# Kernel tuning notes

Measured on AMD Instinct MI355X. Metric: run time of the kernel, lower is better.

Reference implementation:

```python
import jax, jax.numpy as jnp
import numpy as np

N = 50000
E = 800000
F0, F1, F2 = 256, 128, 64
EPS = 1e-5


def setup_inputs() -> dict:
    key = jax.random.key(0)
    ks = jax.random.split(key, 20)
    x = jax.random.normal(ks[0], (N, F0), dtype=jnp.float32)
    src = jax.random.randint(ks[1], (E,), 0, N)
    dst = jax.random.randint(ks[2], (E,), 0, N)
    edge_index = jnp.stack([src, dst]).astype(jnp.int64)

    def lin(k, fi, fo):
        s = 1.0 / np.sqrt(fi)
        k1, k2 = jax.random.split(k)
        W = jax.random.uniform(k1, (fi, fo), minval=-s, maxval=s, dtype=jnp.float32)
        b = jax.random.uniform(k2, (fo,), minval=-s, maxval=s, dtype=jnp.float32)
        return W, b

    We1, be1 = lin(ks[3], F0, F1)
    We2, be2 = lin(ks[4], F1, F2)
    Wd1, bd1 = lin(ks[5], F2, F1)
    Wd2, bd2 = lin(ks[6], F1, F0)
    return {
        'x': x, 'edge_index': edge_index,
        'We1': We1, 'be1': be1, 'g1': jnp.ones((F1,)), 'bb1': jnp.zeros((F1,)),
        'We2': We2, 'be2': be2, 'g2': jnp.ones((F2,)), 'bb2': jnp.zeros((F2,)),
        'Wd1': Wd1, 'bd1': bd1, 'g3': jnp.ones((F1,)), 'bb3': jnp.zeros((F1,)),
        'Wd2': Wd2, 'bd2': bd2, 'g4': jnp.ones((F0,)), 'bb4': jnp.zeros((F0,)),
    }


def _gcn(x, W, b, src, dst, dinv_src_dst, dinv_self):
    # PyG GCNConv: linear first, then sym-normalized propagation with self-loops
    h = x @ W + b                               # [N, Fout]
    msg = h[src] * dinv_src_dst[:, None]        # [E, Fout]
    out = jax.ops.segment_sum(msg, dst, num_segments=N)
    return out + h * dinv_self[:, None]         # self-loop term


def _bn(x, g, b):
    # BatchNorm1d training-mode: biased batch stats over node dim
    m = jnp.mean(x, axis=0)
    v = jnp.mean(jnp.square(x - m), axis=0)
    return g * (x - m) * jax.lax.rsqrt(v + EPS) + b


def reference(x, edge_index, We1, be1, g1, bb1, We2, be2, g2, bb2,
              Wd1, bd1, g3, bb3, Wd2, bd2, g4, bb4):
    src, dst = edge_index[0], edge_index[1]
    deg = jnp.zeros((N,), x.dtype).at[dst].add(1.0) + 1.0  # in-degree + self-loop
    dinv = jax.lax.rsqrt(deg)
    dsd = dinv[src] * dinv[dst]
    dself = dinv * dinv

    relu = jax.nn.relu
    # Encoder block 0 (outer i==0): relu(GCN), relu(BN)
    h = relu(_gcn(x, We1, be1, src, dst, dsd, dself))
    h = relu(_bn(h, g1, bb1))
    enc1 = h
    # Encoder block 1 (outer i==1 == len(inner)-1): relu(GCN), BN (no relu)
    h = relu(_gcn(h, We2, be2, src, dst, dsd, dself))
    h = _bn(h, g2, bb2)
    enc2 = h
    # Decoder block 0: relu(GCN), relu(BN)
    h = relu(_gcn(h, Wd1, bd1, src, dst, dsd, dself))
    h = relu(_bn(h, g3, bb3))
    # Decoder block 1 (i==1): relu(GCN), BN (no relu)
    h = relu(_gcn(h, Wd2, bd2, src, dst, dsd, dself))
    h = _bn(h, g4, bb4)
    # AE returns (reconstruction, encoded_embeddings)
    return h, enc1, enc2
```

## Files before the change

kernel.cpp:

```cpp
#include <hip/hip_runtime.h>

#define N_NODES 50000
#define F0 256
#define F1 128
#define F2 64
#define BN_EPS 1e-5f

typedef float f32x4 __attribute__((ext_vector_type(4)));
typedef __bf16 bf16x8 __attribute__((ext_vector_type(8)));
typedef unsigned short ushort8v __attribute__((ext_vector_type(8)));

__device__ __forceinline__ float bflo(unsigned v) { return __uint_as_float(v << 16); }
__device__ __forceinline__ float bfhi(unsigned v) { return __uint_as_float(v & 0xFFFF0000u); }
__device__ __forceinline__ unsigned short f2bf(float f) {
  unsigned u = __float_as_uint(f);
  u += 0x7FFFu + ((u >> 16) & 1u);
  return (unsigned short)(u >> 16);
}
__device__ __forceinline__ void split2(float a, unsigned short& hi, unsigned short& lo) {
  hi = f2bf(a);
  float hf = __uint_as_float((unsigned)hi << 16);
  lo = f2bf(a - hf);
}
__device__ __forceinline__ int rdl(int v, int l) { return __builtin_amdgcn_readlane(v, l); }
__device__ __forceinline__ float rdlf(float v, int l) {
  return __uint_as_float((unsigned)__builtin_amdgcn_readlane(__float_as_int(v), l));
}

__global__ void count_dst(const int* __restrict__ dst, int* __restrict__ counts, int E) {
  int e = blockIdx.x * blockDim.x + threadIdx.x;
  if (e < E) atomicAdd(&counts[dst[e]], 1);
}

__global__ __launch_bounds__(256) void scan_blocks(const int* __restrict__ counts,
                                                   int* __restrict__ offs,
                                                   int* __restrict__ bsum,
                                                   float* __restrict__ dinv) {
  __shared__ int s_w[4];
  const int tid = threadIdx.x, lane = tid & 63, wid = tid >> 6;
  const int base = blockIdx.x * 1024 + tid * 4;
  int v0 = 0, v1 = 0, v2 = 0, v3 = 0;
  if (base + 3 < N_NODES) {
    int4 v = *(const int4*)(counts + base);
    v0 = v.x; v1 = v.y; v2 = v.z; v3 = v.w;
  } else if (base < N_NODES) {
    v0 = counts[base];
    if (base + 1 < N_NODES) v1 = counts[base + 1];
    if (base + 2 < N_NODES) v2 = counts[base + 2];
  }
  if (base < N_NODES) {
    dinv[base] = rsqrtf((float)v0 + 1.0f);
    if (base + 1 < N_NODES) dinv[base + 1] = rsqrtf((float)v1 + 1.0f);
    if (base + 2 < N_NODES) dinv[base + 2] = rsqrtf((float)v2 + 1.0f);
    if (base + 3 < N_NODES) dinv[base + 3] = rsqrtf((float)v3 + 1.0f);
  }
  int t = v0 + v1 + v2 + v3;
  int incl = t;
#pragma unroll
  for (int d = 1; d < 64; d <<= 1) {
    int x = __shfl_up(incl, d);
    if (lane >= d) incl += x;
  }
  if (lane == 63) s_w[wid] = incl;
  __syncthreads();
  int woff = 0;
#pragma unroll
  for (int j = 0; j < 4; j++)
    if (j < wid) woff += s_w[j];
  int p = woff + incl - t;
  if (base < N_NODES) offs[base] = p;
  p += v0;
  if (base + 1 < N_NODES) offs[base + 1] = p;
  p += v1;
  if (base + 2 < N_NODES) offs[base + 2] = p;
  p += v2;
  if (base + 3 < N_NODES) offs[base + 3] = p;
  if (tid == 255) bsum[blockIdx.x] = woff + incl;
}

__global__ void scan_tops(int* __restrict__ bsum, int* __restrict__ offs, int nblk) {
  int lane = threadIdx.x;
  int v = (lane < nblk) ? bsum[lane] : 0;
  int incl = v;
#pragma unroll
  for (int d = 1; d < 64; d <<= 1) {
    int x = __shfl_up(incl, d);
    if (lane >= d) incl += x;
  }
  if (lane < nblk) bsum[lane] = incl - v;
  if (lane == 63) offs[N_NODES] = incl;
}

__global__ __launch_bounds__(256) void scan_add(int* __restrict__ offs,
                                                const int* __restrict__ bsum) {
  const int add = bsum[blockIdx.x];
  const int base = blockIdx.x * 1024 + threadIdx.x * 4;
  if (base + 3 < N_NODES) {
    int4 v = *(const int4*)(offs + base);
    v.x += add; v.y += add; v.z += add; v.w += add;
    *(int4*)(offs + base) = v;
  } else if (base < N_NODES) {
    offs[base] += add;
    if (base + 1 < N_NODES) offs[base + 1] += add;
    if (base + 2 < N_NODES) offs[base + 2] += add;
  }
}

__global__ void fill_csr(const int* __restrict__ src, const int* __restrict__ dst,
                         const int* __restrict__ offs, int* __restrict__ cursor,
                         const float* __restrict__ dinv,
                         int* __restrict__ csr_src, float* __restrict__ csr_w, int E) {
  int e = blockIdx.x * blockDim.x + threadIdx.x;
  if (e < E) {
    int s = src[e], d = dst[e];
    int p = offs[d] + atomicAdd(&cursor[d], 1);
    csr_src[p] = s;
    csr_w[p] = dinv[s] * dinv[d];
  }
}

__global__ void compute_rowsum(const int* __restrict__ offs, const float* __restrict__ csr_w,
                               const float* __restrict__ dinv, float* __restrict__ rowsum) {
  int i = blockIdx.x * blockDim.x + threadIdx.x;
  if (i < N_NODES) {
    float s = dinv[i] * dinv[i];
    int e1 = offs[i + 1];
    for (int e = offs[i]; e < e1; e++) s += csr_w[e];
    rowsum[i] = s;
  }
}

__device__ __forceinline__ void wt_one(const float* W, unsigned short* Wh, unsigned short* Wl,
                                       int K, int N, int idx) {
  int k = idx / N, n = idx - k * N;
  unsigned short h, l;
  split2(W[idx], h, l);
  Wh[(size_t)n * K + k] = h;
  Wl[(size_t)n * K + k] = l;
}

__global__ void convert_weights(const float* __restrict__ We1, const float* __restrict__ We2,
                                const float* __restrict__ Wd1, const float* __restrict__ Wd2,
                                unsigned short* W1h, unsigned short* W1l,
                                unsigned short* W2h, unsigned short* W2l,
                                unsigned short* W3h, unsigned short* W3l,
                                unsigned short* W4h, unsigned short* W4l) {
  int idx = blockIdx.x * blockDim.x + threadIdx.x;
  if (idx < 32768) {
    wt_one(We1, W1h, W1l, 256, 128, idx);
  } else if (idx < 40960) {
    wt_one(We2, W2h, W2l, 128, 64, idx - 32768);
  } else if (idx < 49152) {
    wt_one(Wd1, W3h, W3l, 64, 128, idx - 40960);
  } else if (idx < 81920) {
    wt_one(Wd2, W4h, W4l, 128, 256, idx - 49152);
  }
}

template <int BN, bool STATS, bool AF32>
__global__ __launch_bounds__(256) void mfma_gemm_split(
    const unsigned short* __restrict__ Ahi, const unsigned short* __restrict__ Alo,
    const float* __restrict__ Af,
    const unsigned short* __restrict__ Whi, const unsigned short* __restrict__ Wlo,
    const float* __restrict__ bias, const float* __restrict__ rowsum,
    unsigned short* __restrict__ Cb, float* __restrict__ Cf,
    float* __restrict__ stat, int M, int K, int N) {
  constexpr int BM = 128;
  constexpr int MT = (BN == 128) ? 4 : 2;
  constexpr int NT = 4;
  __shared__ __align__(16) unsigned short AsH[4][BM][8];
  __shared__ __align__(16) unsigned short AsL[4][BM][8];
  __shared__ __align__(16) unsigned short BsH[4][BN][8];
  __shared__ __align__(16) unsigned short BsL[4][BN][8];
  const int tid = threadIdx.x;
  const int lane = tid & 63, wid = tid >> 6;
  const int quad = lane >> 4, ln = lane & 15;
  const int m0 = blockIdx.x * BM;
  const int n0 = blockIdx.y * BN;
  const int wm = (BN == 128) ? (wid & 1) * 64 : wid * 32;
  const int wn = (BN == 128) ? (wid >> 1) * 64 : 0;
  f32x4 acc[MT][NT] = {};

  const int arow = tid >> 2, aseg = tid & 3;
  for (int k0 = 0; k0 < K; k0 += 32) {
#pragma unroll
    for (int i = 0; i < 2; i++) {
      int row = arow + i * 64;
      int gm = m0 + row;
      if (AF32) {
        float4 u0 = make_float4(0.f, 0.f, 0.f, 0.f), u1 = u0;
        if (gm < M) {
          u0 = *(const float4*)(Af + (size_t)gm * K + k0 + aseg * 8);
          u1 = *(const float4*)(Af + (size_t)gm * K + k0 + aseg * 8 + 4);
        }
        ushort4 h0, l0, h1, l1;
        split2(u0.x, h0.x, l0.x); split2(u0.y, h0.y, l0.y);
        split2(u0.z, h0.z, l0.z); split2(u0.w, h0.w, l0.w);
        split2(u1.x, h1.x, l1.x); split2(u1.y, h1.y, l1.y);
        split2(u1.z, h1.z, l1.z); split2(u1.w, h1.w, l1.w);
        *(ushort4*)(&AsH[aseg][row][0]) = h0;
        *(ushort4*)(&AsH[aseg][row][4]) = h1;
        *(ushort4*)(&AsL[aseg][row][0]) = l0;
        *(ushort4*)(&AsL[aseg][row][4]) = l1;
      } else {
        ushort8v vh = {0, 0, 0, 0, 0, 0, 0, 0};
        ushort8v vl = {0, 0, 0, 0, 0, 0, 0, 0};
        if (gm < M) {
          vh = *(const ushort8v*)(Ahi + (size_t)gm * K + k0 + aseg * 8);
          vl = *(const ushort8v*)(Alo + (size_t)gm * K + k0 + aseg * 8);
        }
        *(ushort8v*)(&AsH[aseg][row][0]) = vh;
        *(ushort8v*)(&AsL[aseg][row][0]) = vl;
      }
    }
#pragma unroll
    for (int i = 0; i < BN / 64; i++) {
      int n = arow + i * 64;
      *(ushort8v*)(&BsH[aseg][n][0]) =
          *(const ushort8v*)(Whi + (size_t)(n0 + n) * K + k0 + aseg * 8);
      *(ushort8v*)(&BsL[aseg][n][0]) =
          *(const ushort8v*)(Wlo + (size_t)(n0 + n) * K + k0 + aseg * 8);
    }
    __syncthreads();
    bf16x8 ah[MT], al[MT], bh[NT], bl[NT];
#pragma unroll
    for (int mt = 0; mt < MT; mt++) {
      ah[mt] = *(const bf16x8*)(&AsH[quad][wm + mt * 16 + ln][0]);
      al[mt] = *(const bf16x8*)(&AsL[quad][wm + mt * 16 + ln][0]);
    }
#pragma unroll
    for (int nt = 0; nt < NT; nt++) {
      bh[nt] = *(const bf16x8*)(&BsH[quad][wn + nt * 16 + ln][0]);
      bl[nt] = *(const bf16x8*)(&BsL[quad][wn + nt * 16 + ln][0]);
    }
#pragma unroll
    for (int mt = 0; mt < MT; mt++)
#pragma unroll
      for (int nt = 0; nt < NT; nt++) {
        acc[mt][nt] = __builtin_amdgcn_mfma_f32_16x16x32_bf16(ah[mt], bl[nt], acc[mt][nt], 0, 0, 0);
        acc[mt][nt] = __builtin_amdgcn_mfma_f32_16x16x32_bf16(al[mt], bh[nt], acc[mt][nt], 0, 0, 0);
        acc[mt][nt] = __builtin_amdgcn_mfma_f32_16x16x32_bf16(ah[mt], bh[nt], acc[mt][nt], 0, 0, 0);
      }
    __syncthreads();
  }

  if (!STATS) {
#pragma unroll
    for (int nt = 0; nt < NT; nt++) {
      int gn = n0 + wn + nt * 16 + ln;
      float bv = bias[gn];
#pragma unroll
      for (int mt = 0; mt < MT; mt++) {
#pragma unroll
        for (int r = 0; r < 4; r++) {
          int gm = m0 + wm + mt * 16 + quad * 4 + r;
          if (gm < M) Cb[(size_t)gm * N + gn] = f2bf(acc[mt][nt][r] + bv);
        }
      }
    }
  } else {
    float rs[MT][4];
#pragma unroll
    for (int mt = 0; mt < MT; mt++)
#pragma unroll
      for (int r = 0; r < 4; r++) {
        int gm = m0 + wm + mt * 16 + quad * 4 + r;
        rs[mt][r] = (gm < M) ? rowsum[gm] : 0.f;
      }
#pragma unroll
    for (int nt = 0; nt < NT; nt++) {
      int gn = n0 + wn + nt * 16 + ln;
      float bv = bias[gn];
      float ls = 0.f, lq = 0.f;
#pragma unroll
      for (int mt = 0; mt < MT; mt++) {
#pragma unroll
        for (int r = 0; r < 4; r++) {
          int gm = m0 + wm + mt * 16 + quad * 4 + r;
          if (gm < M) {
            float v = fmaxf(fmaf(bv, rs[mt][r], acc[mt][nt][r]), 0.f);
            Cf[(size_t)gm * N + gn] = v;
            ls += v;
            lq = fmaf(v, v, lq);
          }
        }
      }
      ls += __shfl_xor(ls, 16); ls += __shfl_xor(ls, 32);
      lq += __shfl_xor(lq, 16); lq += __shfl_xor(lq, 32);
      if (quad == 0) {
        atomicAdd(&stat[gn], ls);
        atomicAdd(&stat[256 + gn], lq);
      }
    }
  }
}

template <bool RELU_STATS, bool OUT_SPLIT>
__global__ __launch_bounds__(256) void agg128_rl(
    const unsigned short* __restrict__ hb, const int* __restrict__ offs,
    const int* __restrict__ csr_src, const float* __restrict__ csr_w,
    const float* __restrict__ dinv, float* __restrict__ outf,
    unsigned short* __restrict__ outhi, unsigned short* __restrict__ outlo,
    float* __restrict__ stat) {
  const int tid = threadIdx.x;
  const int lane = tid & 63;
  const int widx = tid >> 6;
  const int half = lane >> 5;
  const int hl = lane & 31;
  const int nwaves = gridDim.x * 4;
  float ls0 = 0.f, ls1 = 0.f, ls2 = 0.f, ls3 = 0.f;
  float lq0 = 0.f, lq1 = 0.f, lq2 = 0.f, lq3 = 0.f;

  for (int node = blockIdx.x * 4 + widx; node < N_NODES; node += nwaves) {
    const int e0 = __builtin_amdgcn_readfirstlane(offs[node]);
    const int e1 = __builtin_amdgcn_readfirstlane(offs[node + 1]);
    float a0 = 0.f, a1 = 0.f, a2 = 0.f, a3 = 0.f;
    for (int e = e0; e < e1; e += 64) {
      const int cnt = min(64, e1 - e);
      int idx = 0;
      float wt = 0.f;
      if (lane < cnt) {
        idx = csr_src[e + lane];
        wt = csr_w[e + lane];
      }
      const int nb = (cnt + 15) & ~15;
      for (int j = 0; j < nb; j += 16) {
#pragma unroll
        for (int u = 0; u < 8; u++) {
          int sa = rdl(idx, j + 2 * u);
          int sb = rdl(idx, j + 2 * u + 1);
          float wa = rdlf(wt, j + 2 * u);
          float wb = rdlf(wt, j + 2 * u + 1);
          int s = half ? sb : sa;
          float w = half ? wb : wa;
          uint2 v = *(const uint2*)(hb + (size_t)s * 128 + hl * 4);
          a0 = fmaf(bflo(v.x), w, a0);
          a1 = fmaf(bfhi(v.x), w, a1);
          a2 = fmaf(bflo(v.y), w, a2);
          a3 = fmaf(bfhi(v.y), w, a3);
        }
      }
    }
    a0 += __shfl_xor(a0, 32);
    a1 += __shfl_xor(a1, 32);
    a2 += __shfl_xor(a2, 32);
    a3 += __shfl_xor(a3, 32);
    float di = dinv[node];
    float ds = di * di;
    uint2 vs = *(const uint2*)(hb + (size_t)node * 128 + hl * 4);
    a0 = fmaf(bflo(vs.x), ds, a0);
    a1 = fmaf(bfhi(vs.x), ds, a1);
    a2 = fmaf(bflo(vs.y), ds, a2);
    a3 = fmaf(bfhi(vs.y), ds, a3);
    if (RELU_STATS) {
      a0 = fmaxf(a0, 0.f);
      a1 = fmaxf(a1, 0.f);
      a2 = fmaxf(a2, 0.f);
      a3 = fmaxf(a3, 0.f);
      if (half == 0) {
        ls0 += a0; ls1 += a1; ls2 += a2; ls3 += a3;
        lq0 = fmaf(a0, a0, lq0);
        lq1 = fmaf(a1, a1, lq1);
        lq2 = fmaf(a2, a2, lq2);
        lq3 = fmaf(a3, a3, lq3);
      }
    }
    if (half == 0) {
      if (OUT_SPLIT) {
        unsigned short h0, l0, h1, l1, h2, l2, h3, l3;
        split2(a0, h0, l0);
        split2(a1, h1, l1);
        split2(a2, h2, l2);
        split2(a3, h3, l3);
        ushort4 hv, lv;
        hv.x = h0; hv.y = h1; hv.z = h2; hv.w = h3;
        lv.x = l0; lv.y = l1; lv.z = l2; lv.w = l3;
        *(ushort4*)(outhi + (size_t)node * 128 + hl * 4) = hv;
        *(ushort4*)(outlo + (size_t)node * 128 + hl * 4) = lv;
      } else {
        *(float4*)(outf + (size_t)node * 128 + hl * 4) = make_float4(a0, a1, a2, a3);
      }
    }
  }

  if (RELU_STATS) {
    __shared__ float red[4][128];
    if (half == 0) {
      red[widx][hl * 4 + 0] = ls0;
      red[widx][hl * 4 + 1] = ls1;
      red[widx][hl * 4 + 2] = ls2;
      red[widx][hl * 4 + 3] = ls3;
    }
    __syncthreads();
    if (tid < 128) {
      atomicAdd(&stat[tid], red[0][tid] + red[1][tid] + red[2][tid] + red[3][tid]);
    }
    __syncthreads();
    if (half == 0) {
      red[widx][hl * 4 + 0] = lq0;
      red[widx][hl * 4 + 1] = lq1;
      red[widx][hl * 4 + 2] = lq2;
      red[widx][hl * 4 + 3] = lq3;
    }
    __syncthreads();
    if (tid < 128) {
      atomicAdd(&stat[256 + tid], red[0][tid] + red[1][tid] + red[2][tid] + red[3][tid]);
    }
  }
}

template <bool RELU_STATS, bool OUT_SPLIT>
__global__ __launch_bounds__(256) void agg64_rl(
    const unsigned short* __restrict__ hb, const int* __restrict__ offs,
    const int* __restrict__ csr_src, const float* __restrict__ csr_w,
    const float* __restrict__ dinv, float* __restrict__ outf,
    unsigned short* __restrict__ outhi, unsigned short* __restrict__ outlo,
    float* __restrict__ stat) {
  const int tid = threadIdx.x;
  const int lane = tid & 63;
  const int widx = tid >> 6;
  const int ql = lane & 15;
  const int nwaves = gridDim.x * 4;
  float ls0 = 0.f, ls1 = 0.f, ls2 = 0.f, ls3 = 0.f;
  float lq0 = 0.f, lq1 = 0.f, lq2 = 0.f, lq3 = 0.f;

  for (int node = blockIdx.x * 4 + widx; node < N_NODES; node += nwaves) {
    const int e0 = __builtin_amdgcn_readfirstlane(offs[node]);
    const int e1 = __builtin_amdgcn_readfirstlane(offs[node + 1]);
    float a0 = 0.f, a1 = 0.f, a2 = 0.f, a3 = 0.f;
    for (int e = e0; e < e1; e += 64) {
      const int cnt = min(64, e1 - e);
      int idx = 0;
      float wt = 0.f;
      if (lane < cnt) {
        idx = csr_src[e + lane];
        wt = csr_w[e + lane];
      }
      const int nb = (cnt + 31) & ~31;
      for (int j = 0; j < nb; j += 32) {
#pragma unroll
        for (int u = 0; u < 8; u++) {
          int s0 = rdl(idx, j + 4 * u + 0);
          int s1 = rdl(idx, j + 4 * u + 1);
          int s2 = rdl(idx, j + 4 * u + 2);
          int s3 = rdl(idx, j + 4 * u + 3);
          float w0 = rdlf(wt, j + 4 * u + 0);
          float w1 = rdlf(wt, j + 4 * u + 1);
          float w2 = rdlf(wt, j + 4 * u + 2);
          float w3 = rdlf(wt, j + 4 * u + 3);
          int sx = (lane & 16) ? s1 : s0;
          int sy = (lane & 16) ? s3 : s2;
          int s = (lane & 32) ? sy : sx;
          float wx = (lane & 16) ? w1 : w0;
          float wy = (lane & 16) ? w3 : w2;
          float w = (lane & 32) ? wy : wx;
          uint2 v = *(const uint2*)(hb + (size_t)s * 64 + ql * 4);
          a0 = fmaf(bflo(v.x), w, a0);
          a1 = fmaf(bfhi(v.x), w, a1);
          a2 = fmaf(bflo(v.y), w, a2);
          a3 = fmaf(bfhi(v.y), w, a3);
        }
      }
    }
    a0 += __shfl_xor(a0, 16); a0 += __shfl_xor(a0, 32);
    a1 += __shfl_xor(a1, 16); a1 += __shfl_xor(a1, 32);
    a2 += __shfl_xor(a2, 16); a2 += __shfl_xor(a2, 32);
    a3 += __shfl_xor(a3, 16); a3 += __shfl_xor(a3, 32);
    float di = dinv[node];
    float ds = di * di;
    uint2 vs = *(const uint2*)(hb + (size_t)node * 64 + ql * 4);
    a0 = fmaf(bflo(vs.x), ds, a0);
    a1 = fmaf(bfhi(vs.x), ds, a1);
    a2 = fmaf(bflo(vs.y), ds, a2);
    a3 = fmaf(bfhi(vs.y), ds, a3);
    if (RELU_STATS) {
      a0 = fmaxf(a0, 0.f);
      a1 = fmaxf(a1, 0.f);
      a2 = fmaxf(a2, 0.f);
      a3 = fmaxf(a3, 0.f);
      if (lane < 16) {
        ls0 += a0; ls1 += a1; ls2 += a2; ls3 += a3;
        lq0 = fmaf(a0, a0, lq0);
        lq1 = fmaf(a1, a1, lq1);
        lq2 = fmaf(a2, a2, lq2);
        lq3 = fmaf(a3, a3, lq3);
      }
    }
    if (lane < 16) {
      if (OUT_SPLIT) {
        unsigned short h0, l0, h1, l1, h2, l2, h3, l3;
        split2(a0, h0, l0);
        split2(a1, h1, l1);
        split2(a2, h2, l2);
        split2(a3, h3, l3);
        ushort4 hv, lv;
        hv.x = h0; hv.y = h1; hv.z = h2; hv.w = h3;
        lv.x = l0; lv.y = l1; lv.z = l2; lv.w = l3;
        *(ushort4*)(outhi + (size_t)node * 64 + ql * 4) = hv;
        *(ushort4*)(outlo + (size_t)node * 64 + ql * 4) = lv;
      } else {
        *(float4*)(outf + (size_t)node * 64 + ql * 4) = make_float4(a0, a1, a2, a3);
      }
    }
  }

  if (RELU_STATS) {
    __shared__ float red[4][64];
    if (lane < 16) {
      red[widx][ql * 4 + 0] = ls0;
      red[widx][ql * 4 + 1] = ls1;
      red[widx][ql * 4 + 2] = ls2;
      red[widx][ql * 4 + 3] = ls3;
    }
    __syncthreads();
    if (tid < 64) {
      atomicAdd(&stat[tid], red[0][tid] + red[1][tid] + red[2][tid] + red[3][tid]);
    }
    __syncthreads();
    if (lane < 16) {
      red[widx][ql * 4 + 0] = lq0;
      red[widx][ql * 4 + 1] = lq1;
      red[widx][ql * 4 + 2] = lq2;
      red[widx][ql * 4 + 3] = lq3;
    }
    __syncthreads();
    if (tid < 64) {
      atomicAdd(&stat[256 + tid], red[0][tid] + red[1][tid] + red[2][tid] + red[3][tid]);
    }
  }
}

template <int F, bool RELU, bool WF32, bool WB16, bool WSPLIT>
__global__ __launch_bounds__(256) void bn_apply_f(const float* __restrict__ a,
                                                  const float* __restrict__ stat,
                                                  const float* __restrict__ g,
                                                  const float* __restrict__ bb,
                                                  float* __restrict__ outf,
                                                  unsigned short* __restrict__ outb,
                                                  unsigned short* __restrict__ outhi,
                                                  unsigned short* __restrict__ outlo) {
  __shared__ float s_scale[F], s_shift[F];
  const int tid = threadIdx.x;
  if (tid < F) {
    const float invN = 1.0f / (float)N_NODES;
    float mean = stat[tid] * invN;
    float var = fmaxf(stat[256 + tid] * invN - mean * mean, 0.f);
    float inv = rsqrtf(var + BN_EPS);
    float sc = g[tid] * inv;
    s_scale[tid] = sc;
    s_shift[tid] = bb[tid] - mean * sc;
  }
  __syncthreads();
  constexpr int C4 = F / 4;
  const int total = N_NODES * C4;
  for (int idx = blockIdx.x * blockDim.x + tid; idx < total; idx += gridDim.x * blockDim.x) {
    int c4 = idx % C4;
    float4 v = ((const float4*)a)[idx];
    float4 s = *(float4*)&s_scale[c4 * 4];
    float4 sh = *(float4*)&s_shift[c4 * 4];
    float4 o;
    o.x = fmaf(v.x, s.x, sh.x);
    o.y = fmaf(v.y, s.y, sh.y);
    o.z = fmaf(v.z, s.z, sh.z);
    o.w = fmaf(v.w, s.w, sh.w);
    if (RELU) {
      o.x = fmaxf(o.x, 0.f);
      o.y = fmaxf(o.y, 0.f);
      o.z = fmaxf(o.z, 0.f);
      o.w = fmaxf(o.w, 0.f);
    }
    if (WF32) ((float4*)outf)[idx] = o;
    if (WB16) {
      ushort4 b;
      b.x = f2bf(o.x); b.y = f2bf(o.y); b.z = f2bf(o.z); b.w = f2bf(o.w);
      ((ushort4*)outb)[idx] = b;
    }
    if (WSPLIT) {
      ushort4 h, l;
      split2(o.x, h.x, l.x);
      split2(o.y, h.y, l.y);
      split2(o.z, h.z, l.z);
      split2(o.w, h.w, l.w);
      ((ushort4*)outhi)[idx] = h;
      ((ushort4*)outlo)[idx] = l;
    }
  }
}

extern "C" void kernel_launch(void* const* d_in, const int* in_sizes, int n_in,
                              void* d_out, int out_size, void* d_ws, size_t ws_size,
                              hipStream_t stream) {
  const float* x = (const float*)d_in[0];
  const int* ei = (const int*)d_in[1];
  const int E = in_sizes[1] / 2;
  const int* src = ei;
  const int* dst = ei + E;
  const float* We1 = (const float*)d_in[2];  const float* be1 = (const float*)d_in[3];
  const float* g1  = (const float*)d_in[4];  const float* bb1 = (const float*)d_in[5];
  const float* We2 = (const float*)d_in[6];  const float* be2 = (const float*)d_in[7];
  const float* g2  = (const float*)d_in[8];  const float* bb2 = (const float*)d_in[9];
  const float* Wd1 = (const float*)d_in[10]; const float* bd1 = (const float*)d_in[11];
  const float* g3  = (const float*)d_in[12]; const float* bb3 = (const float*)d_in[13];
  const float* Wd2 = (const float*)d_in[14]; const float* bd2 = (const float*)d_in[15];
  const float* g4  = (const float*)d_in[16]; const float* bb4 = (const float*)d_in[17];

  float* out = (float*)d_out;
  char* ws = (char*)d_ws;
  unsigned short* A0b  = (unsigned short*)(ws + 0);
  unsigned short* A1b  = (unsigned short*)(ws + 12800000);
  unsigned short* C2b  = (unsigned short*)(ws + 32000000);
  unsigned short* G3hi = (unsigned short*)(ws + 0);
  unsigned short* G3lo = (unsigned short*)(ws + 6400000);
  unsigned short* D3b  = (unsigned short*)(ws + 12800000);
  unsigned short* G4hi = (unsigned short*)(ws + 0);
  unsigned short* G4lo = (unsigned short*)(ws + 25600000);
  unsigned short* Wb   = (unsigned short*)(ws + 48000000);
  unsigned short* W1h = Wb;            unsigned short* W1l = W1h + 32768;
  unsigned short* W2h = W1l + 32768;   unsigned short* W2l = W2h + 8192;
  unsigned short* W3h = W2l + 8192;    unsigned short* W3l = W3h + 8192;
  unsigned short* W4h = W3l + 8192;    unsigned short* W4l = W4h + 32768;
  float* B0f  = (float*)(ws + 51200000);
  int*   csrS   = (int*)(ws + 102400000);
  float* csrW   = (float*)(ws + 105600000);
  float* stat4  = (float*)(ws + 108800000);
  int*   bsum   = (int*)(ws + 108808192);
  int*   counts = (int*)(ws + 108810000);
  int*   cursor = (int*)(ws + 109010000);
  int*   offs   = (int*)(ws + 109210000);
  float* dinv   = (float*)(ws + 109410064);
  if (ws_size < 109604160) return;
  float* rowsum = (float*)cursor;

  float* enc1 = out + (size_t)N_NODES * F0;
  float* enc2 = enc1 + (size_t)N_NODES * F1;

  const int EB = (E + 255) / 256;
  const int AGG_GRID = 2048;
  const int MB = (N_NODES + 127) / 128;
  const int SCAN_B = (N_NODES + 1023) / 1024;

  convert_weights<<<320, 256, 0, stream>>>(We1, We2, Wd1, Wd2, W1h, W1l, W2h, W2l,
                                           W3h, W3l, W4h, W4l);
  hipMemsetAsync(counts, 0, 2 * N_NODES * sizeof(int) + 20000, stream);
  hipMemsetAsync(stat4, 0, 4 * 512 * sizeof(float), stream);
  count_dst<<<EB, 256, 0, stream>>>(dst, counts, E);
  scan_blocks<<<SCAN_B, 256, 0, stream>>>(counts, offs, bsum, dinv);
  scan_tops<<<1, 64, 0, stream>>>(bsum, offs, SCAN_B);
  scan_add<<<SCAN_B, 256, 0, stream>>>(offs, bsum);
  fill_csr<<<EB, 256, 0, stream>>>(src, dst, offs, cursor, dinv, csrS, csrW, E);
  compute_rowsum<<<(N_NODES + 255) / 256, 256, 0, stream>>>(offs, csrW, dinv, rowsum);

  mfma_gemm_split<128, false, true><<<dim3(MB, 1), 256, 0, stream>>>(
      nullptr, nullptr, x, W1h, W1l, be1, nullptr, A0b, nullptr, nullptr, N_NODES, F0, F1);
  agg128_rl<true, false><<<AGG_GRID, 256, 0, stream>>>(
      A0b, offs, csrS, csrW, dinv, B0f, nullptr, nullptr, stat4);
  bn_apply_f<F1, true, true, false, false><<<2048, 256, 0, stream>>>(
      B0f, stat4, g1, bb1, enc1, nullptr, nullptr, nullptr);

  mfma_gemm_split<64, false, true><<<dim3(MB, 1), 256, 0, stream>>>(
      nullptr, nullptr, enc1, W2h, W2l, be2, nullptr, A1b, nullptr, nullptr, N_NODES, F1, F2);
  agg64_rl<true, false><<<AGG_GRID, 256, 0, stream>>>(
      A1b, offs, csrS, csrW, dinv, B0f, nullptr, nullptr, stat4 + 512);
  bn_apply_f<F2, false, true, true, false><<<2048, 256, 0, stream>>>(
      B0f, stat4 + 512, g2, bb2, enc2, C2b, nullptr, nullptr);

  agg64_rl<false, true><<<AGG_GRID, 256, 0, stream>>>(
      C2b, offs, csrS, csrW, dinv, nullptr, G3hi, G3lo, nullptr);
  mfma_gemm_split<128, true, false><<<dim3(MB, 1), 256, 0, stream>>>(
      G3hi, G3lo, nullptr, W3h, W3l, bd1, rowsum, nullptr, B0f, stat4 + 1024, N_NODES, F2, F1);
  bn_apply_f<F1, true, false, true, false><<<2048, 256, 0, stream>>>(
      B0f, stat4 + 1024, g3, bb3, nullptr, D3b, nullptr, nullptr);

  agg128_rl<false, true><<<AGG_GRID, 256, 0, stream>>>(
      D3b, offs, csrS, csrW, dinv, nullptr, G4hi, G4lo, nullptr);
  mfma_gemm_split<128, true, false><<<dim3(MB, 2), 256, 0, stream>>>(
      G4hi, G4lo, nullptr, W4h, W4l, bd2, rowsum, nullptr, B0f, stat4 + 1536, N_NODES, F1, F0);
  bn_apply_f<F0, false, true, false, false><<<2048, 256, 0, stream>>>(
      B0f, stat4 + 1536, g4, bb4, out, nullptr, nullptr, nullptr);
}
```

Baseline: 642.6 us.

## Slice bf16 features into 8-wide column panels for cache-resident sparse aggregation

```diff
diff --git a/kernel.cpp b/kernel.cpp
--- a/kernel.cpp
+++ b/kernel.cpp
@@ -21,10 +21,6 @@
   hi = f2bf(a);
   float hf = __uint_as_float((unsigned)hi << 16);
   lo = f2bf(a - hf);
-}
-__device__ __forceinline__ int rdl(int v, int l) { return __builtin_amdgcn_readlane(v, l); }
-__device__ __forceinline__ float rdlf(float v, int l) {
-  return __uint_as_float((unsigned)__builtin_amdgcn_readlane(__float_as_int(v), l));
 }
 
 __global__ void count_dst(const int* __restrict__ dst, int* __restrict__ counts, int E) {
@@ -92,41 +88,39 @@
 }
 
 __global__ __launch_bounds__(256) void scan_add(int* __restrict__ offs,
-                                                const int* __restrict__ bsum) {
+                                                const int* __restrict__ bsum,
+                                                const float* __restrict__ dinv,
+                                                float* __restrict__ rowsum) {
   const int add = bsum[blockIdx.x];
   const int base = blockIdx.x * 1024 + threadIdx.x * 4;
   if (base + 3 < N_NODES) {
     int4 v = *(const int4*)(offs + base);
     v.x += add; v.y += add; v.z += add; v.w += add;
     *(int4*)(offs + base) = v;
+    float4 d = *(const float4*)(dinv + base);
+    float4 r;
+    r.x = d.x * d.x; r.y = d.y * d.y; r.z = d.z * d.z; r.w = d.w * d.w;
+    *(float4*)(rowsum + base) = r;
   } else if (base < N_NODES) {
-    offs[base] += add;
-    if (base + 1 < N_NODES) offs[base + 1] += add;
-    if (base + 2 < N_NODES) offs[base + 2] += add;
+    for (int k = 0; k < 4 && base + k < N_NODES; k++) {
+      offs[base + k] += add;
+      float d = dinv[base + k];
+      rowsum[base + k] = d * d;
+    }
   }
 }
 
 __global__ void fill_csr(const int* __restrict__ src, const int* __restrict__ dst,
                          const int* __restrict__ offs, int* __restrict__ cursor,
                          const float* __restrict__ dinv,
-                         int* __restrict__ csr_src, float* __restrict__ csr_w, int E) {
+                         int2* __restrict__ csrP, float* __restrict__ rowsum, int E) {
   int e = blockIdx.x * blockDim.x + threadIdx.x;
   if (e < E) {
     int s = src[e], d = dst[e];
     int p = offs[d] + atomicAdd(&cursor[d], 1);
-    csr_src[p] = s;
-    csr_w[p] = dinv[s] * dinv[d];
-  }
-}
-
-__global__ void compute_rowsum(const int* __restrict__ offs, const float* __restrict__ csr_w,
-                               const float* __restrict__ dinv, float* __restrict__ rowsum) {
-  int i = blockIdx.x * blockDim.x + threadIdx.x;
-  if (i < N_NODES) {
-    float s = dinv[i] * dinv[i];
-    int e1 = offs[i + 1];
-    for (int e = offs[i]; e < e1; e++) s += csr_w[e];
-    rowsum[i] = s;
+    float w = dinv[s] * dinv[d];
+    csrP[p] = make_int2(s, __float_as_int(w));
+    atomicAdd(&rowsum[d], w);
   }
 }
 
@@ -249,12 +243,14 @@
     for (int nt = 0; nt < NT; nt++) {
       int gn = n0 + wn + nt * 16 + ln;
       float bv = bias[gn];
+      const int slice = gn >> 3, wi = gn & 7;
+      unsigned short* cp = Cb + (size_t)slice * (N_NODES * 8) + wi;
 #pragma unroll
       for (int mt = 0; mt < MT; mt++) {
 #pragma unroll
         for (int r = 0; r < 4; r++) {
           int gm = m0 + wm + mt * 16 + quad * 4 + r;
-          if (gm < M) Cb[(size_t)gm * N + gn] = f2bf(acc[mt][nt][r] + bv);
+          if (gm < M) cp[(size_t)gm * 8] = f2bf(acc[mt][nt][r] + bv);
         }
       }
     }
@@ -295,250 +291,142 @@
   }
 }
 
+
 template <bool RELU_STATS, bool OUT_SPLIT>
-__global__ __launch_bounds__(256) void agg128_rl(
+__device__ __forceinline__ void agg_emit(int node, int s, int chunk, int F,
+                                         float a0, float a1,
+                                         const unsigned short* __restrict__ hbs,
+                                         const float* __restrict__ dinv,
+                                         float* __restrict__ outf,
+                                         unsigned short* __restrict__ outhi,
+                                         unsigned short* __restrict__ outlo,
+                                         float& ls0, float& ls1, float& lq0, float& lq1) {
+  float di = dinv[node];
+  float ds = di * di;
+  unsigned v = *(const unsigned*)(hbs + (size_t)node * 8 + chunk * 2);
+  a0 = fmaf(bflo(v), ds, a0);
+  a1 = fmaf(bfhi(v), ds, a1);
+  if (RELU_STATS) {
+    a0 = fmaxf(a0, 0.f);
+    a1 = fmaxf(a1, 0.f);
+    ls0 += a0; ls1 += a1;
+    lq0 = fmaf(a0, a0, lq0);
+    lq1 = fmaf(a1, a1, lq1);
+  }
+  size_t p = (size_t)node * F + s * 8 + chunk * 2;
+  if (OUT_SPLIT) {
+    unsigned short h0, l0, h1, l1;
+    split2(a0, h0, l0);
+    split2(a1, h1, l1);
+    *(unsigned*)(outhi + p) = (unsigned)h0 | ((unsigned)h1 << 16);
+    *(unsigned*)(outlo + p) = (unsigned)l0 | ((unsigned)l1 << 16);
+  } else {
+    *(float2*)(outf + p) = make_float2(a0, a1);
+  }
+}
+
+template <bool RELU_STATS, bool OUT_SPLIT, int S>
+__global__ __launch_bounds__(256) void agg_sl(
     const unsigned short* __restrict__ hb, const int* __restrict__ offs,
-    const int* __restrict__ csr_src, const float* __restrict__ csr_w,
-    const float* __restrict__ dinv, float* __restrict__ outf,
-    unsigned short* __restrict__ outhi, unsigned short* __restrict__ outlo,
-    float* __restrict__ stat) {
+    const int2* __restrict__ csrP, const float* __restrict__ dinv,
+    float* __restrict__ outf, unsigned short* __restrict__ outhi,
+    unsigned short* __restrict__ outlo, float* __restrict__ stat, int nb) {
   const int tid = threadIdx.x;
   const int lane = tid & 63;
   const int widx = tid >> 6;
-  const int half = lane >> 5;
-  const int hl = lane & 31;
-  const int nwaves = gridDim.x * 4;
-  float ls0 = 0.f, ls1 = 0.f, ls2 = 0.f, ls3 = 0.f;
-  float lq0 = 0.f, lq1 = 0.f, lq2 = 0.f, lq3 = 0.f;
-
-  for (int node = blockIdx.x * 4 + widx; node < N_NODES; node += nwaves) {
-    const int e0 = __builtin_amdgcn_readfirstlane(offs[node]);
-    const int e1 = __builtin_amdgcn_readfirstlane(offs[node + 1]);
-    float a0 = 0.f, a1 = 0.f, a2 = 0.f, a3 = 0.f;
-    for (int e = e0; e < e1; e += 64) {
-      const int cnt = min(64, e1 - e);
-      int idx = 0;
-      float wt = 0.f;
-      if (lane < cnt) {
-        idx = csr_src[e + lane];
-        wt = csr_w[e + lane];
-      }
-      const int nb = (cnt + 15) & ~15;
-      for (int j = 0; j < nb; j += 16) {
-#pragma unroll
-        for (int u = 0; u < 8; u++) {
-          int sa = rdl(idx, j + 2 * u);
-          int sb = rdl(idx, j + 2 * u + 1);
-          float wa = rdlf(wt, j + 2 * u);
-          float wb = rdlf(wt, j + 2 * u + 1);
-          int s = half ? sb : sa;
-          float w = half ? wb : wa;
-          uint2 v = *(const uint2*)(hb + (size_t)s * 128 + hl * 4);
-          a0 = fmaf(bflo(v.x), w, a0);
-          a1 = fmaf(bfhi(v.x), w, a1);
-          a2 = fmaf(bflo(v.y), w, a2);
-          a3 = fmaf(bfhi(v.y), w, a3);
+  const int slot = lane >> 2;
+  const int chunk = lane & 3;
+  const int s = blockIdx.x % S;
+  const int blk = blockIdx.x / S;
+  const int stride = nb * 4;
+  constexpr int F = S * 8;
+  const unsigned short* hbs = hb + (size_t)s * (N_NODES * 8);
+  float ls0 = 0.f, ls1 = 0.f, lq0 = 0.f, lq1 = 0.f;
+
+  for (int base = blk * 4 + widx; base < N_NODES; base += 2 * stride) {
+    const int nA = base, nB = base + stride;
+    const bool hasB = (nB < N_NODES);
+    int eA = __builtin_amdgcn_readfirstlane(offs[nA]);
+    const int eA1 = __builtin_amdgcn_readfirstlane(offs[nA + 1]);
+    int eB = 0, eB1 = 0;
+    if (hasB) {
+      eB = __builtin_amdgcn_readfirstlane(offs[nB]);
+      eB1 = __builtin_amdgcn_readfirstlane(offs[nB + 1]);
+    }
+    float aA0 = 0.f, aA1 = 0.f, aB0 = 0.f, aB1 = 0.f;
+    while (eA < eA1 || eB < eB1) {
+      if (eA < eA1) {
+        int ee = eA + slot;
+        if (ee < eA1) {
+          unsigned long long cw =
+              __builtin_nontemporal_load((const unsigned long long*)&csrP[ee]);
+          int sn = (int)(unsigned)cw;
+          float w = __uint_as_float((unsigned)(cw >> 32));
+          unsigned v = *(const unsigned*)(hbs + (size_t)sn * 8 + chunk * 2);
+          aA0 = fmaf(bflo(v), w, aA0);
+          aA1 = fmaf(bfhi(v), w, aA1);
         }
       }
-    }
-    a0 += __shfl_xor(a0, 32);
-    a1 += __shfl_xor(a1, 32);
-    a2 += __shfl_xor(a2, 32);
-    a3 += __shfl_xor(a3, 32);
-    float di = dinv[node];
-    float ds = di * di;
-    uint2 vs = *(const uint2*)(hb + (size_t)node * 128 + hl * 4);
-    a0 = fmaf(bflo(vs.x), ds, a0);
-    a1 = fmaf(bfhi(vs.x), ds, a1);
-    a2 = fmaf(bflo(vs.y), ds, a2);
-    a3 = fmaf(bfhi(vs.y), ds, a3);
-    if (RELU_STATS) {
-      a0 = fmaxf(a0, 0.f);
-      a1 = fmaxf(a1, 0.f);
-      a2 = fmaxf(a2, 0.f);
-      a3 = fmaxf(a3, 0.f);
-      if (half == 0) {
-        ls0 += a0; ls1 += a1; ls2 += a2; ls3 += a3;
-        lq0 = fmaf(a0, a0, lq0);
-        lq1 = fmaf(a1, a1, lq1);
-        lq2 = fmaf(a2, a2, lq2);
-        lq3 = fmaf(a3, a3, lq3);
-      }
-    }
-    if (half == 0) {
-      if (OUT_SPLIT) {
-        unsigned short h0, l0, h1, l1, h2, l2, h3, l3;
-        split2(a0, h0, l0);
-        split2(a1, h1, l1);
-        split2(a2, h2, l2);
-        split2(a3, h3, l3);
-        ushort4 hv, lv;
-        hv.x = h0; hv.y = h1; hv.z = h2; hv.w = h3;
-        lv.x = l0; lv.y = l1; lv.z = l2; lv.w = l3;
-        *(ushort4*)(outhi + (size_t)node * 128 + hl * 4) = hv;
-        *(ushort4*)(outlo + (size_t)node * 128 + hl * 4) = lv;
-      } else {
-        *(float4*)(outf + (size_t)node * 128 + hl * 4) = make_float4(a0, a1, a2, a3);
-      }
+      if (eB < eB1) {
+        int ee = eB + slot;
+        if (ee < eB1) {
+          unsigned long long cw =
+              __builtin_nontemporal_load((const unsigned long long*)&csrP[ee]);
+          int sn = (int)(unsigned)cw;
+          float w = __uint_as_float((unsigned)(cw >> 32));
+          unsigned v = *(const unsigned*)(hbs + (size_t)sn * 8 + chunk * 2);
+          aB0 = fmaf(bflo(v), w, aB0);
+          aB1 = fmaf(bfhi(v), w, aB1);
+        }
+      }
+      eA += 16;
+      eB += 16;
+    }
+#pragma unroll
+    for (int d = 4; d < 64; d <<= 1) {
+      aA0 += __shfl_xor(aA0, d);
+      aA1 += __shfl_xor(aA1, d);
+    }
+    if (hasB) {
+#pragma unroll
+      for (int d = 4; d < 64; d <<= 1) {
+        aB0 += __shfl_xor(aB0, d);
+        aB1 += __shfl_xor(aB1, d);
+      }
+    }
+    if (slot == 0) {
+      agg_emit<RELU_STATS, OUT_SPLIT>(nA, s, chunk, F, aA0, aA1, hbs, dinv, outf, outhi, outlo,
+                                      ls0, ls1, lq0, lq1);
+      if (hasB)
+        agg_emit<RELU_STATS, OUT_SPLIT>(nB, s, chunk, F, aB0, aB1, hbs, dinv, outf, outhi, outlo,
+                                        ls0, ls1, lq0, lq1);
     }
   }
 
   if (RELU_STATS) {
-    __shared__ float red[4][128];
-    if (half == 0) {
-      red[widx][hl * 4 + 0] = ls0;
-      red[widx][hl * 4 + 1] = ls1;
-      red[widx][hl * 4 + 2] = ls2;
-      red[widx][hl * 4 + 3] = ls3;
+    __shared__ float red[4][16];
+    if (slot == 0) {
+      red[widx][chunk * 2 + 0] = ls0;
+      red[widx][chunk * 2 + 1] = ls1;
+      red[widx][8 + chunk * 2 + 0] = lq0;
+      red[widx][8 + chunk * 2 + 1] = lq1;
     }
     __syncthreads();
-    if (tid < 128) {
-      atomicAdd(&stat[tid], red[0][tid] + red[1][tid] + red[2][tid] + red[3][tid]);
-    }
-    __syncthreads();
-    if (half == 0) {
-      red[widx][hl * 4 + 0] = lq0;
-      red[widx][hl * 4 + 1] = lq1;
-      red[widx][hl * 4 + 2] = lq2;
-      red[widx][hl * 4 + 3] = lq3;
-    }
-    __syncthreads();
-    if (tid < 128) {
-      atomicAdd(&stat[256 + tid], red[0][tid] + red[1][tid] + red[2][tid] + red[3][tid]);
-    }
-  }
-}
-
-template <bool RELU_STATS, bool OUT_SPLIT>
-__global__ __launch_bounds__(256) void agg64_rl(
-    const unsigned short* __restrict__ hb, const int* __restrict__ offs,
-    const int* __restrict__ csr_src, const float* __restrict__ csr_w,
-    const float* __restrict__ dinv, float* __restrict__ outf,
-    unsigned short* __restrict__ outhi, unsigned short* __restrict__ outlo,
-    float* __restrict__ stat) {
-  const int tid = threadIdx.x;
-  const int lane = tid & 63;
-  const int widx = tid >> 6;
-  const int ql = lane & 15;
-  const int nwaves = gridDim.x * 4;
-  float ls0 = 0.f, ls1 = 0.f, ls2 = 0.f, ls3 = 0.f;
-  float lq0 = 0.f, lq1 = 0.f, lq2 = 0.f, lq3 = 0.f;
-
-  for (int node = blockIdx.x * 4 + widx; node < N_NODES; node += nwaves) {
-    const int e0 = __builtin_amdgcn_readfirstlane(offs[node]);
-    const int e1 = __builtin_amdgcn_readfirstlane(offs[node + 1]);
-    float a0 = 0.f, a1 = 0.f, a2 = 0.f, a3 = 0.f;
-    for (int e = e0; e < e1; e += 64) {
-      const int cnt = min(64, e1 - e);
-      int idx = 0;
-      float wt = 0.f;
-      if (lane < cnt) {
-        idx = csr_src[e + lane];
-        wt = csr_w[e + lane];
-      }
-      const int nb = (cnt + 31) & ~31;
-      for (int j = 0; j < nb; j += 32) {
-#pragma unroll
-        for (int u = 0; u < 8; u++) {
-          int s0 = rdl(idx, j + 4 * u + 0);
-          int s1 = rdl(idx, j + 4 * u + 1);
-          int s2 = rdl(idx, j + 4 * u + 2);
-          int s3 = rdl(idx, j + 4 * u + 3);
-          float w0 = rdlf(wt, j + 4 * u + 0);
-          float w1 = rdlf(wt, j + 4 * u + 1);
-          float w2 = rdlf(wt, j + 4 * u + 2);
-          float w3 = rdlf(wt, j + 4 * u + 3);
-          int sx = (lane & 16) ? s1 : s0;
-          int sy = (lane & 16) ? s3 : s2;
-          int s = (lane & 32) ? sy : sx;
-          float wx = (lane & 16) ? w1 : w0;
-          float wy = (lane & 16) ? w3 : w2;
-          float w = (lane & 32) ? wy : wx;
-          uint2 v = *(const uint2*)(hb + (size_t)s * 64 + ql * 4);
-          a0 = fmaf(bflo(v.x), w, a0);
-          a1 = fmaf(bfhi(v.x), w, a1);
-          a2 = fmaf(bflo(v.y), w, a2);
-          a3 = fmaf(bfhi(v.y), w, a3);
-        }
-      }
-    }
-    a0 += __shfl_xor(a0, 16); a0 += __shfl_xor(a0, 32);
-    a1 += __shfl_xor(a1, 16); a1 += __shfl_xor(a1, 32);
-    a2 += __shfl_xor(a2, 16); a2 += __shfl_xor(a2, 32);
-    a3 += __shfl_xor(a3, 16); a3 += __shfl_xor(a3, 32);
-    float di = dinv[node];
-    float ds = di * di;
-    uint2 vs = *(const uint2*)(hb + (size_t)node * 64 + ql * 4);
-    a0 = fmaf(bflo(vs.x), ds, a0);
-    a1 = fmaf(bfhi(vs.x), ds, a1);
-    a2 = fmaf(bflo(vs.y), ds, a2);
-    a3 = fmaf(bfhi(vs.y), ds, a3);
-    if (RELU_STATS) {
-      a0 = fmaxf(a0, 0.f);
-      a1 = fmaxf(a1, 0.f);
-      a2 = fmaxf(a2, 0.f);
-      a3 = fmaxf(a3, 0.f);
-      if (lane < 16) {
-        ls0 += a0; ls1 += a1; ls2 += a2; ls3 += a3;
-        lq0 = fmaf(a0, a0, lq0);
-        lq1 = fmaf(a1, a1, lq1);
-        lq2 = fmaf(a2, a2, lq2);
-        lq3 = fmaf(a3, a3, lq3);
-      }
-    }
-    if (lane < 16) {
-      if (OUT_SPLIT) {
-        unsigned short h0, l0, h1, l1, h2, l2, h3, l3;
-        split2(a0, h0, l0);
-        split2(a1, h1, l1);
-        split2(a2, h2, l2);
-        split2(a3, h3, l3);
-        ushort4 hv, lv;
-        hv.x = h0; hv.y = h1; hv.z = h2; hv.w = h3;
-        lv.x = l0; lv.y = l1; lv.z = l2; lv.w = l3;
-        *(ushort4*)(outhi + (size_t)node * 64 + ql * 4) = hv;
-        *(ushort4*)(outlo + (size_t)node * 64 + ql * 4) = lv;
-      } else {
-        *(float4*)(outf + (size_t)node * 64 + ql * 4) = make_float4(a0, a1, a2, a3);
-      }
-    }
-  }
-
-  if (RELU_STATS) {
-    __shared__ float red[4][64];
-    if (lane < 16) {
-      red[widx][ql * 4 + 0] = ls0;
-      red[widx][ql * 4 + 1] = ls1;
-      red[widx][ql * 4 + 2] = ls2;
-      red[widx][ql * 4 + 3] = ls3;
-    }
-    __syncthreads();
-    if (tid < 64) {
-      atomicAdd(&stat[tid], red[0][tid] + red[1][tid] + red[2][tid] + red[3][tid]);
-    }
-    __syncthreads();
-    if (lane < 16) {
-      red[widx][ql * 4 + 0] = lq0;
-      red[widx][ql * 4 + 1] = lq1;
-      red[widx][ql * 4 + 2] = lq2;
-      red[widx][ql * 4 + 3] = lq3;
-    }
-    __syncthreads();
-    if (tid < 64) {
-      atomicAdd(&stat[256 + tid], red[0][tid] + red[1][tid] + red[2][tid] + red[3][tid]);
-    }
-  }
-}
-
-template <int F, bool RELU, bool WF32, bool WB16, bool WSPLIT>
+    if (tid < 16) {
+      float v = red[0][tid] + red[1][tid] + red[2][tid] + red[3][tid];
+      int f = s * 8 + (tid & 7);
+      atomicAdd(&stat[(tid >> 3) * 256 + f], v);
+    }
+  }
+}
+
+template <int F, bool RELU, bool WF32, bool WB16>
 __global__ __launch_bounds__(256) void bn_apply_f(const float* __restrict__ a,
                                                   const float* __restrict__ stat,
                                                   const float* __restrict__ g,
                                                   const float* __restrict__ bb,
                                                   float* __restrict__ outf,
-                                                  unsigned short* __restrict__ outb,
-                                                  unsigned short* __restrict__ outhi,
-                                                  unsigned short* __restrict__ outlo) {
+                                                  unsigned short* __restrict__ outb) {
   __shared__ float s_scale[F], s_shift[F];
   const int tid = threadIdx.x;
   if (tid < F) {
@@ -555,6 +443,7 @@
   const int total = N_NODES * C4;
   for (int idx = blockIdx.x * blockDim.x + tid; idx < total; idx += gridDim.x * blockDim.x) {
     int c4 = idx % C4;
+    int node = idx / C4;
     float4 v = ((const float4*)a)[idx];
     float4 s = *(float4*)&s_scale[c4 * 4];
     float4 sh = *(float4*)&s_shift[c4 * 4];
@@ -573,16 +462,8 @@
     if (WB16) {
       ushort4 b;
       b.x = f2bf(o.x); b.y = f2bf(o.y); b.z = f2bf(o.z); b.w = f2bf(o.w);
-      ((ushort4*)outb)[idx] = b;
-    }
-    if (WSPLIT) {
-      ushort4 h, l;
-      split2(o.x, h.x, l.x);
-      split2(o.y, h.y, l.y);
-      split2(o.z, h.z, l.z);
-      split2(o.w, h.w, l.w);
-      ((ushort4*)outhi)[idx] = h;
-      ((ushort4*)outlo)[idx] = l;
+      int slice = c4 >> 1, half = c4 & 1;
+      ((ushort4*)outb)[(size_t)slice * (N_NODES * 2) + (size_t)node * 2 + half] = b;
     }
   }
 }
@@ -620,8 +501,7 @@
   unsigned short* W3h = W2l + 8192;    unsigned short* W3l = W3h + 8192;
   unsigned short* W4h = W3l + 8192;    unsigned short* W4l = W4h + 32768;
   float* B0f  = (float*)(ws + 51200000);
-  int*   csrS   = (int*)(ws + 102400000);
-  float* csrW   = (float*)(ws + 105600000);
+  int2*  csrP   = (int2*)(ws + 102400000);
   float* stat4  = (float*)(ws + 108800000);
   int*   bsum   = (int*)(ws + 108808192);
   int*   counts = (int*)(ws + 108810000);
@@ -629,52 +509,50 @@
   int*   offs   = (int*)(ws + 109210000);
   float* dinv   = (float*)(ws + 109410064);
   if (ws_size < 109604160) return;
-  float* rowsum = (float*)cursor;
+  float* rowsum = (float*)counts;
 
   float* enc1 = out + (size_t)N_NODES * F0;
   float* enc2 = enc1 + (size_t)N_NODES * F1;
 
   const int EB = (E + 255) / 256;
-  const int AGG_GRID = 2048;
   const int MB = (N_NODES + 127) / 128;
   const int SCAN_B = (N_NODES + 1023) / 1024;
 
   convert_weights<<<320, 256, 0, stream>>>(We1, We2, Wd1, Wd2, W1h, W1l, W2h, W2l,
                                            W3h, W3l, W4h, W4l);
-  hipMemsetAsync(counts, 0, 2 * N_NODES * sizeof(int) + 20000, stream);
+  hipMemsetAsync(counts, 0, 400000, stream);
   hipMemsetAsync(stat4, 0, 4 * 512 * sizeof(float), stream);
   count_dst<<<EB, 256, 0, stream>>>(dst, counts, E);
   scan_blocks<<<SCAN_B, 256, 0, stream>>>(counts, offs, bsum, dinv);
   scan_tops<<<1, 64, 0, stream>>>(bsum, offs, SCAN_B);
-  scan_add<<<SCAN_B, 256, 0, stream>>>(offs, bsum);
-  fill_csr<<<EB, 256, 0, stream>>>(src, dst, offs, cursor, dinv, csrS, csrW, E);
-  compute_rowsum<<<(N_NODES + 255) / 256, 256, 0, stream>>>(offs, csrW, dinv, rowsum);
+  scan_add<<<SCAN_B, 256, 0, stream>>>(offs, bsum, dinv, rowsum);
+  fill_csr<<<EB, 256, 0, stream>>>(src, dst, offs, cursor, dinv, csrP, rowsum, E);
 
   mfma_gemm_split<128, false, true><<<dim3(MB, 1), 256, 0, stream>>>(
       nullptr, nullptr, x, W1h, W1l, be1, nullptr, A0b, nullptr, nullptr, N_NODES, F0, F1);
-  agg128_rl<true, false><<<AGG_GRID, 256, 0, stream>>>(
-      A0b, offs, csrS, csrW, dinv, B0f, nullptr, nullptr, stat4);
-  bn_apply_f<F1, true, true, false, false><<<2048, 256, 0, stream>>>(
-      B0f, stat4, g1, bb1, enc1, nullptr, nullptr, nullptr);
+  agg_sl<true, false, 16><<<16 * 128, 256, 0, stream>>>(
+      A0b, offs, csrP, dinv, B0f, nullptr, nullptr, stat4, 128);
+  bn_apply_f<F1, true, true, false><<<2048, 256, 0, stream>>>(
+      B0f, stat4, g1, bb1, enc1, nullptr);
 
   mfma_gemm_split<64, false, true><<<dim3(MB, 1), 256, 0, stream>>>(
       nullptr, nullptr, enc1, W2h, W2l, be2, nullptr, A1b, nullptr, nullptr, N_NODES, F1, F2);
-  agg64_rl<true, false><<<AGG_GRID, 256, 0, stream>>>(
-      A1b, offs, csrS, csrW, dinv, B0f, nullptr, nullptr, stat4 + 512);
-  bn_apply_f<F2, false, true, true, false><<<2048, 256, 0, stream>>>(
-      B0f, stat4 + 512, g2, bb2, enc2, C2b, nullptr, nullptr);
-
-  agg64_rl<false, true><<<AGG_GRID, 256, 0, stream>>>(
-      C2b, offs, csrS, csrW, dinv, nullptr, G3hi, G3lo, nullptr);
+  agg_sl<true, false, 8><<<8 * 256, 256, 0, stream>>>(
+      A1b, offs, csrP, dinv, B0f, nullptr, nullptr, stat4 + 512, 256);
+  bn_apply_f<F2, false, true, true><<<2048, 256, 0, stream>>>(
+      B0f, stat4 + 512, g2, bb2, enc2, C2b);
+
+  agg_sl<false, true, 8><<<8 * 256, 256, 0, stream>>>(
+      C2b, offs, csrP, dinv, nullptr, G3hi, G3lo, nullptr, 256);
   mfma_gemm_split<128, true, false><<<dim3(MB, 1), 256, 0, stream>>>(
       G3hi, G3lo, nullptr, W3h, W3l, bd1, rowsum, nullptr, B0f, stat4 + 1024, N_NODES, F2, F1);
-  bn_apply_f<F1, true, false, true, false><<<2048, 256, 0, stream>>>(
-      B0f, stat4 + 1024, g3, bb3, nullptr, D3b, nullptr, nullptr);
-
-  agg128_rl<false, true><<<AGG_GRID, 256, 0, stream>>>(
-      D3b, offs, csrS, csrW, dinv, nullptr, G4hi, G4lo, nullptr);
+  bn_apply_f<F1, true, false, true><<<2048, 256, 0, stream>>>(
+      B0f, stat4 + 1024, g3, bb3, nullptr, D3b);
+
+  agg_sl<false, true, 16><<<16 * 128, 256, 0, stream>>>(
+      D3b, offs, csrP, dinv, nullptr, G4hi, G4lo, nullptr, 128);
   mfma_gemm_split<128, true, false><<<dim3(MB, 2), 256, 0, stream>>>(
       G4hi, G4lo, nullptr, W4h, W4l, bd2, rowsum, nullptr, B0f, stat4 + 1536, N_NODES, F1, F0);
-  bn_apply_f<F0, false, true, false, false><<<2048, 256, 0, stream>>>(
-      B0f, stat4 + 1536, g4, bb4, out, nullptr, nullptr, nullptr);
-}
+  bn_apply_f<F0, false, true, false><<<2048, 256, 0, stream>>>(
+      B0f, stat4 + 1536, g4, bb4, out, nullptr);
+}
```

Result: slower. 1.188 ms (+84.8%).
